# Kernel optimization log

Measured on AMD Instinct MI355X. Metric: run time of the kernel, lower is better.

Reference implementation:

```python
import jax, jax.numpy as jnp
import numpy as np

LAMBDA_TV = 0.01
RHO = 1.0
MAX_ITER = 10
CG_ITER = 10


def _fft2c(x):
    # x: (B, 2, H, W) real/imag stacked -> centered ortho FFT, same layout
    xc = x[:, 0] + 1j * x[:, 1]
    kc = jnp.fft.fftshift(
        jnp.fft.fft2(jnp.fft.ifftshift(xc, axes=(-2, -1)), norm='ortho'),
        axes=(-2, -1))
    return jnp.stack([kc.real, kc.imag], axis=1)


def _ifft2c(x):
    xc = x[:, 0] + 1j * x[:, 1]
    ic = jnp.fft.fftshift(
        jnp.fft.ifft2(jnp.fft.ifftshift(xc, axes=(-2, -1)), norm='ortho'),
        axes=(-2, -1))
    return jnp.stack([ic.real, ic.imag], axis=1)


def _gradient(x):
    # forward differences, zero at the far boundary; cat along channel dim
    dx = jnp.concatenate([x[..., 1:] - x[..., :-1], jnp.zeros_like(x[..., :1])], axis=-1)
    dy = jnp.concatenate([x[..., 1:, :] - x[..., :-1, :], jnp.zeros_like(x[..., :1, :])], axis=-2)
    return jnp.concatenate([dx, dy], axis=1)


def _divergence(p):
    # Faithful to the original: only uses channels 0 and 1 of p -> (B,1,H,W)
    px, py = p[:, 0:1], p[:, 1:2]
    div_x = jnp.concatenate(
        [px[..., 0:1], px[..., 1:-1] - px[..., :-2], -px[..., -2:-1]], axis=-1)
    div_y = jnp.concatenate(
        [py[..., 0:1, :], py[..., 1:-1, :] - py[..., :-2, :], -py[..., -2:-1, :]], axis=-2)
    return div_x + div_y


def soft_threshold(x, t):
    return jnp.sign(x) * jnp.maximum(jnp.abs(x) - t, 0.0)


def _cg_solve(x0, b, mask):
    # Solves (F^H M F + rho * D^H D) x = b with early-stop semantics of the original
    def A(z):
        return _ifft2c(mask * _fft2c(z)) - RHO * _divergence(_gradient(z))

    r0 = b - A(x0)
    rsold0 = jnp.sum(r0 * r0)

    def step(carry, _):
        x, r, p, rsold, done = carry
        Ap = A(p)
        alpha = rsold / (jnp.sum(p * Ap) + 1e-12)
        xn = x + alpha * p
        rn = r - alpha * Ap
        rsnew = jnp.sum(rn * rn)
        stop = rsnew < 1e-10
        pn = rn + (rsnew / rsold) * p
        x = jnp.where(done, x, xn)
        r = jnp.where(done, r, rn)
        p = jnp.where(done | stop, p, pn)
        rsold = jnp.where(done | stop, rsold, rsnew)
        done = done | stop
        return (x, r, p, rsold, done), None

    init = (x0, r0, r0, rsold0, jnp.array(False))
    (x, _, _, _, _), _ = jax.lax.scan(step, init, None, length=CG_ITER)
    return x


def reference(y, mask):
    x0 = _ifft2c(y)
    u0 = _gradient(x0)
    v0 = jnp.zeros_like(u0)
    b_data = _ifft2c(mask * y)  # constant across outer iterations
    thresh = LAMBDA_TV / RHO

    def step(carry, _):
        x, u, v, done, count, pres_l, dres_l = carry
        b = b_data + RHO * _divergence(u - v)
        xn = _cg_solve(x, b, mask)
        g = _gradient(xn)
        un = soft_threshold(g + v, thresh)
        vn = v + g - un
        pres = jnp.linalg.norm(g - un)
        dres = jnp.linalg.norm(RHO * _divergence(un - u))
        stop = (pres < 1e-4) & (dres < 1e-4)
        x = jnp.where(done, x, xn)
        u = jnp.where(done, u, un)
        v = jnp.where(done, v, vn)
        pres_l = jnp.where(done, pres_l, pres)
        dres_l = jnp.where(done, dres_l, dres)
        count = count + (1 - done.astype(jnp.int32))
        done = done | stop
        return (x, u, v, done, count, pres_l, dres_l), None

    init = (x0, u0, v0, jnp.array(False), jnp.array(0, jnp.int32),
            jnp.array(0.0, x0.dtype), jnp.array(0.0, x0.dtype))
    (x, _, _, _, count, pres, dres), _ = jax.lax.scan(step, init, None, length=MAX_ITER)
    return x, count, pres, dres


def setup_inputs() -> dict:
    key = jax.random.key(0)
    k1, k2 = jax.random.split(key)
    B, H, W = 4, 320, 320
    y = jax.random.normal(k1, (B, 2, H, W), dtype=jnp.float32)
    mask = (jax.random.uniform(k2, (B, 1, H, W)) < 0.3).astype(jnp.float32)
    return {"y": y, "mask": mask}
```

## Files before the change

### kernel.cpp

```cpp
#include <hip/hip_runtime.h>
#include <math.h>

#define DEVFN __device__ __forceinline__

namespace {

constexpr int NW = 320, NH = 320, NHW = NW * NH, NB = 4;
constexpr int NC2 = 2 * NHW;
constexpr int GRID = NB * NH;
constexpr int NTHR = 320;
constexpr float THRESHc = 0.01f;

struct C2 { float x, y; };
DEVFN C2 cmul(C2 a, C2 b) { return C2{a.x * b.x - a.y * b.y, a.x * b.y + a.y * b.x}; }

template <int SIGN>
DEVFN C2 TW(const float2* tw, int m) {
  float2 t = tw[m];
  return C2{t.x, (SIGN < 0) ? t.y : -t.y};
}

DEVFN int swzcol(int bid) { return (bid & 7) * (GRID / 8) + (bid >> 3); }

DEVFN void wavebar() {
  __builtin_amdgcn_wave_barrier();
  asm volatile("" ::: "memory");
}

template <int SIGN, bool MASKED>
__device__ void fftp(const float2* IN, float2* OUT, float2* SCR, const float2* tw, int t,
                     const float* __restrict__ misRow) {
  const int q = t >> 6, n1 = t & 63;
  float2* lo = SCR + q * 128;
  float2* hi = lo + 64;
  float mval = 1.f;
  if (MASKED) mval = misRow[5 * n1 + q];
  C2 acc;
  {
    float2 v0 = IN[n1];
    acc.x = v0.x; acc.y = v0.y;
#pragma unroll
    for (int n2 = 1; n2 < 5; n2++) {
      float2 v = IN[n1 + 64 * n2];
      C2 w = TW<SIGN>(tw, 64 * ((n2 * q) % 5));
      acc.x += v.x * w.x - v.y * w.y;
      acc.y += v.x * w.y + v.y * w.x;
    }
    acc = cmul(acc, TW<SIGN>(tw, n1 * q));
  }
  lo[n1] = make_float2(acc.x, acc.y);
  wavebar();
  {
    C2 s{0.f, 0.f};
    int rr = n1 & 3, base = n1 >> 2;
#pragma unroll
    for (int p = 0; p < 4; p++) {
      float2 v = lo[base + 16 * p];
      C2 w = TW<SIGN>(tw, 80 * ((p * rr) & 3));
      s.x += v.x * w.x - v.y * w.y;
      s.y += v.x * w.y + v.y * w.x;
    }
    hi[n1] = make_float2(s.x, s.y);
  }
  wavebar();
  {
    C2 s{0.f, 0.f};
    int rr = n1 & 15, base = ((n1 >> 4) << 2) + (n1 & 3);
#pragma unroll
    for (int p = 0; p < 4; p++) {
      float2 v = hi[base + 16 * p];
      C2 w = TW<SIGN>(tw, 20 * ((p * rr) & 15));
      s.x += v.x * w.x - v.y * w.y;
      s.y += v.x * w.y + v.y * w.x;
    }
    lo[n1] = make_float2(s.x, s.y);
  }
  wavebar();
  {
    C2 s{0.f, 0.f};
    int base = n1 & 15;
#pragma unroll
    for (int p = 0; p < 4; p++) {
      float2 v = lo[base + 16 * p];
      C2 w = TW<SIGN>(tw, 5 * ((p * n1) & 63));
      s.x += v.x * w.x - v.y * w.y;
      s.y += v.x * w.y + v.y * w.x;
    }
    acc = s;
  }
  if (MASKED) { acc.x *= mval; acc.y *= mval; }
  OUT[5 * n1 + q] = make_float2(acc.x, acc.y);
  __syncthreads();
}

DEVFN float Gfunc2(const float2* __restrict__ z, int b, int h, int w) {
  const float2* zz = z + b * NHW;
  int hw = h * NW + w;
  float divx, divy;
  if (w == 0) {
    divx = zz[hw + 1].x - zz[hw].x;
  } else if (w < NW - 1) {
    divx = (zz[hw + 1].x - zz[hw].x) - (zz[hw].x - zz[hw - 1].x);
  } else {
    divx = -(zz[hw].x - zz[hw - 1].x);
  }
  if (h == 0) {
    divy = (w < NW - 1) ? zz[hw + 1].y - zz[hw].y : 0.f;
  } else if (h < NH - 1) {
    float a = (w < NW - 1) ? zz[hw + 1].y - zz[hw].y : 0.f;
    float bb = (w < NW - 1) ? zz[hw - NW + 1].y - zz[hw - NW].y : 0.f;
    divy = a - bb;
  } else {
    divy = -((w < NW - 1) ? zz[hw - NW + 1].y - zz[hw - NW].y : 0.f);
  }
  return divx + divy;
}

DEVFN float divUV(const float* __restrict__ u, const float* __restrict__ v, int b, int h, int w) {
  const float* u0 = u + (b * 4 + 0) * NHW; const float* v0 = v + (b * 4 + 0) * NHW;
  const float* u1 = u + (b * 4 + 1) * NHW; const float* v1 = v + (b * 4 + 1) * NHW;
  int hw = h * NW + w;
  float divx, divy;
  if (w == 0)          divx = u0[hw] - v0[hw];
  else if (w < NW - 1) divx = (u0[hw] - v0[hw]) - (u0[hw - 1] - v0[hw - 1]);
  else                 divx = -(u0[hw - 1] - v0[hw - 1]);
  if (h == 0)          divy = u1[hw] - v1[hw];
  else if (h < NH - 1) divy = (u1[hw] - v1[hw]) - (u1[hw - NW] - v1[hw - NW]);
  else                 divy = -(u1[hw - NW] - v1[hw - NW]);
  return divx + divy;
}

DEVFN double shflxd(double v, int m) {
  union { double d; int i[2]; } a; a.d = v;
  a.i[0] = __shfl_xor(a.i[0], m, 64);
  a.i[1] = __shfl_xor(a.i[1], m, 64);
  return a.d;
}
DEVFN double waveRed(double v) {
#pragma unroll
  for (int m = 32; m; m >>= 1) v += shflxd(v, m);
  return v;
}

__device__ double redParts(const double* __restrict__ part, double* sdot, int t) {
  double v = part[t] + part[t + 320] + part[t + 640] + part[t + 960];
  v = waveRed(v);
  if ((t & 63) == 0) sdot[t >> 6] = v;
  __syncthreads();
  double s = sdot[0] + sdot[1] + sdot[2] + sdot[3] + sdot[4];
  __syncthreads();
  return s;
}

__device__ void blockDot1(double a, double* sdot, int t, double* outp) {
  a = waveRed(a);
  if ((t & 63) == 0) sdot[t >> 6] = a;
  __syncthreads();
  if (t == 0) *outp = sdot[0] + sdot[1] + sdot[2] + sdot[3] + sdot[4];
  __syncthreads();
}

__device__ void blockDot3(double a, double b, double c, double* sdot, int t,
                          double* o0, double* o1, double* o2, int bid) {
  a = waveRed(a); b = waveRed(b); c = waveRed(c);
  int wv = t >> 6;
  if ((t & 63) == 0) { sdot[wv * 3] = a; sdot[wv * 3 + 1] = b; sdot[wv * 3 + 2] = c; }
  __syncthreads();
  if (t == 0) {
    double s0 = 0, s1 = 0, s2 = 0;
#pragma unroll
    for (int w2 = 0; w2 < 5; w2++) { s0 += sdot[w2 * 3]; s1 += sdot[w2 * 3 + 1]; s2 += sdot[w2 * 3 + 2]; }
    o0[bid] = s0; o1[bid] = s1; o2[bid] = s2;
  }
  __syncthreads();
}

#define FFTK_SHARED                                     \
  __shared__ float2 sA[320];                            \
  __shared__ float2 sB[320];                            \
  __shared__ float2 sS[640];                            \
  __shared__ float2 stw[320];                           \
  __shared__ double sdot[16];                           \
  (void)sdot;                                           \
  const int t = threadIdx.x;                            \
  const int bid = blockIdx.x;                           \
  stw[t] = twg[t];


__global__ __launch_bounds__(NTHR) void k_init(const float* __restrict__ mask,
                                               float* __restrict__ misT, float2* __restrict__ tw) {
  int t = threadIdx.x, bid = blockIdx.x;
  if (bid == 0) {
    double ang = -2.0 * 3.14159265358979323846 * (double)t / 320.0;
    tw[t] = make_float2((float)cos(ang), (float)sin(ang));
  }
  int i = bid * NTHR + t;
  int b = i / NHW, hw = i % NHW, h = hw / NW, w = hw % NW;
  int hs = (h + 160) % 320, ws = (w + 160) % 320;
  misT[b * NHW + w * NW + h] = mask[b * NHW + hs * NW + ws] * (1.0f / 102400.0f);
}

__global__ __launch_bounds__(NTHR) void k0a(const float* __restrict__ y, const float* __restrict__ mask,
                                            float2* __restrict__ t1, float2* __restrict__ t2,
                                            const float2* __restrict__ twg) {
  FFTK_SHARED
  const int gb = bid / NH, gl = bid % NH;
  const int rowBase = gb * NC2 + gl * NW;
  float sgn = (t & 1) ? -1.f : 1.f;
  sA[t] = make_float2(sgn * y[rowBase + t], sgn * y[rowBase + NHW + t]);
  __syncthreads();
  fftp<1, false>(sA, sB, sS, stw, t, nullptr);
  {
    float2 v = sB[t];
    t1[gb * NHW + gl * NW + t] = make_float2(sgn * v.x, sgn * v.y);
  }
  float m = mask[gb * NHW + gl * NW + t];
  sA[t] = make_float2(sgn * m * y[rowBase + t], sgn * m * y[rowBase + NHW + t]);
  __syncthreads();
  fftp<1, false>(sA, sB, sS, stw, t, nullptr);
  {
    float2 v = sB[t];
    t2[gb * NHW + gl * NW + t] = make_float2(sgn * v.x, sgn * v.y);
  }
}

__global__ __launch_bounds__(NTHR) void k0b(const float2* __restrict__ t1, const float2* __restrict__ t2,
                                            float2* __restrict__ x2, float2* __restrict__ bdata2,
                                            const float2* __restrict__ twg) {
  FFTK_SHARED
  const int wid = swzcol(bid);
  const int gb = wid / NH, gl = wid % NH;
  float sgn = (t & 1) ? -1.f : 1.f;
  {
    float2 v = t1[gb * NHW + t * NW + gl];
    sA[t] = make_float2(sgn * v.x, sgn * v.y);
  }
  __syncthreads();
  fftp<1, false>(sA, sB, sS, stw, t, nullptr);
  {
    float2 v = sB[t];
    float s = sgn * (1.f / 320.f);
    x2[gb * NHW + t * NW + gl] = make_float2(v.x * s, v.y * s);
  }
  {
    float2 v = t2[gb * NHW + t * NW + gl];
    sA[t] = make_float2(sgn * v.x, sgn * v.y);
  }
  __syncthreads();
  fftp<1, false>(sA, sB, sS, stw, t, nullptr);
  {
    float2 v = sB[t];
    float s = sgn * (1.f / 320.f);
    bdata2[gb * NHW + t * NW + gl] = make_float2(v.x * s, v.y * s);
  }
}

__global__ __launch_bounds__(NTHR) void ka0(const float2* __restrict__ x2, float2* __restrict__ xc2,
                                            float* __restrict__ u, float* __restrict__ v,
                                            float2* __restrict__ t1, const float2* __restrict__ twg) {
  FFTK_SHARED
  const int gb = bid / NH, gl = bid % NH;
  {
    int i = bid * NTHR + t;
    int b = i / NHW, hw = i % NHW, h = hw / NW, w = hw % NW;
    const float2* zz = x2 + b * NHW;
    float2 z0 = zz[hw];
    float g0 = 0, g1 = 0, g2 = 0, g3 = 0;
    if (w < NW - 1) { float2 zr = zz[hw + 1]; g0 = zr.x - z0.x; g1 = zr.y - z0.y; }
    if (h < NH - 1) { float2 zd = zz[hw + NW]; g2 = zd.x - z0.x; g3 = zd.y - z0.y; }
    int b4 = b * 4 * NHW;
    u[b4 + hw] = g0;           v[b4 + hw] = 0.f;
    u[b4 + NHW + hw] = g1;     v[b4 + NHW + hw] = 0.f;
    u[b4 + 2 * NHW + hw] = g2; v[b4 + 2 * NHW + hw] = 0.f;
    u[b4 + 3 * NHW + hw] = g3; v[b4 + 3 * NHW + hw] = 0.f;
  }
  int idx = gb * NHW + gl * NW + t;
  float2 xv = x2[idx];
  xc2[idx] = xv;
  sA[t] = xv;
  __syncthreads();
  fftp<-1, false>(sA, sB, sS, stw, t, nullptr);
  t1[idx] = sB[t];
}

__global__ __launch_bounds__(NTHR) void kb(float2* __restrict__ t1, const float* __restrict__ misT,
                                           const float* __restrict__ un, const float* __restrict__ vn,
                                           float* __restrict__ u, float* __restrict__ v,
                                           const double* __restrict__ pPaPrev, const double* __restrict__ pPbPrev,
                                           double* __restrict__ hist_pres, double* __restrict__ hist_dres,
                                           const float2* __restrict__ twg, int it) {
  FFTK_SHARED
  const int wid = swzcol(bid);
  const int gb = wid / NH, gl = wid % NH;
  if (it > 0) {
    double ppa = redParts(pPaPrev, sdot, t);
    double ppb = redParts(pPbPrev, sdot, t);
    if (bid == 0 && t == 0) { hist_pres[it - 1] = ppa; hist_dres[it - 1] = ppb; }
    bool doneA = false;
    for (int j = 0; j <= it - 2; j++) {
      float pr = sqrtf((float)hist_pres[j]), dr = sqrtf((float)hist_dres[j]);
      doneA |= (pr < 1e-4f && dr < 1e-4f);
    }
    if (!doneA) {
      for (int i = wid * NTHR + t; i < NB * 4 * NHW; i += GRID * NTHR) { u[i] = un[i]; v[i] = vn[i]; }
    }
  }
  sA[t] = t1[gb * NHW + t * NW + gl];
  __syncthreads();
  fftp<-1, true>(sA, sB, sS, stw, t, misT + gb * NHW + gl * NW);
  fftp<1, false>(sB, sA, sS, stw, t, nullptr);
  t1[gb * NHW + t * NW + gl] = sA[t];
}

__global__ __launch_bounds__(NTHR) void kcd(float2* __restrict__ t1, const float2* __restrict__ x2,
                                            const float* __restrict__ u, const float* __restrict__ v,
                                            const float2* __restrict__ bdata2, float2* __restrict__ r2,
                                            float2* __restrict__ p2, double* __restrict__ pRS,
                                            const float2* __restrict__ twg) {
  FFTK_SHARED
  const int gb = bid / NH, gl = bid % NH;
  const int idx = gb * NHW + gl * NW + t;
  sA[t] = t1[idx];
  __syncthreads();
  fftp<1, false>(sA, sB, sS, stw, t, nullptr);
  float2 Av = sB[t];
  float G = Gfunc2(x2, gb, gl, t);
  float d = divUV(u, v, gb, gl, t);
  float2 bd = bdata2[idx];
  float rr = (bd.x + d) - (Av.x - G);
  float ri = (bd.y + d) - (Av.y - G);
  float2 rv = make_float2(rr, ri);
  r2[idx] = rv; p2[idx] = rv;
  double acc = (double)rr * rr + (double)ri * ri;
  blockDot1(acc, sdot, t, &pRS[bid]);
  sA[t] = rv;
  __syncthreads();
  fftp<-1, false>(sA, sB, sS, stw, t, nullptr);
  t1[idx] = sB[t];
}

__global__ __launch_bounds__(NTHR) void kd(float2* __restrict__ xc2, float2* __restrict__ r2,
                                           float2* __restrict__ p2, const float2* __restrict__ Ap2,
                                           float2* __restrict__ t1, const double* __restrict__ pRS,
                                           const double* __restrict__ pD0, const double* __restrict__ pD1,
                                           const double* __restrict__ pD2, double* __restrict__ hist_rs,
                                           const float2* __restrict__ twg, int k) {
  FFTK_SHARED
  const int gb = bid / NH, gl = bid % NH;
  const int idx = gb * NHW + gl * NW + t;
  double pAp = redParts(pD0, sdot, t);
  double rAp = redParts(pD1, sdot, t);
  double A2  = redParts(pD2, sdot, t);
  double rsold = (k == 1) ? redParts(pRS, sdot, t) : hist_rs[k - 2];
  float alpha = (float)rsold / ((float)pAp + 1e-12f);
  double rsnew = rsold - 2.0 * (double)alpha * rAp + (double)alpha * (double)alpha * A2;
  if (bid == 0 && t == 0) hist_rs[k - 1] = rsnew;
  bool doneIn = false;
  for (int j = 0; j <= k - 2; j++) doneIn |= ((float)hist_rs[j] < 1e-10f);
  bool stop = ((float)rsnew < 1e-10f);
  bool doneP = doneIn || stop;
  float beta = (float)rsnew / (float)rsold;
  float2 pv = p2[idx], rv = r2[idx], av = Ap2[idx], xv = xc2[idx];
  if (!doneIn) {
    xv.x += alpha * pv.x; xv.y += alpha * pv.y;
    rv.x -= alpha * av.x; rv.y -= alpha * av.y;
  }
  float2 pn = doneP ? pv : make_float2(rv.x + beta * pv.x, rv.y + beta * pv.y);
  xc2[idx] = xv; r2[idx] = rv; p2[idx] = pn;
  sA[t] = pn;
  __syncthreads();
  fftp<-1, false>(sA, sB, sS, stw, t, nullptr);
  t1[idx] = sB[t];
}

__global__ __launch_bounds__(NTHR) void ke(float2* __restrict__ t1, const float* __restrict__ misT,
                                           const float2* __restrict__ twg) {
  FFTK_SHARED
  const int wid = swzcol(bid);
  const int gb = wid / NH, gl = wid % NH;
  sA[t] = t1[gb * NHW + t * NW + gl];
  __syncthreads();
  fftp<-1, true>(sA, sB, sS, stw, t, misT + gb * NHW + gl * NW);
  fftp<1, false>(sB, sA, sS, stw, t, nullptr);
  t1[gb * NHW + t * NW + gl] = sA[t];
}

__global__ __launch_bounds__(NTHR) void kf(const float2* __restrict__ t1, const float2* __restrict__ p2,
                                           const float2* __restrict__ r2, float2* __restrict__ Ap2,
                                           double* __restrict__ pD0, double* __restrict__ pD1,
                                           double* __restrict__ pD2, const float2* __restrict__ twg) {
  FFTK_SHARED
  const int gb = bid / NH, gl = bid % NH;
  const int idx = gb * NHW + gl * NW + t;
  sA[t] = t1[idx];
  __syncthreads();
  fftp<1, false>(sA, sB, sS, stw, t, nullptr);
  float2 Av = sB[t];
  float G = Gfunc2(p2, gb, gl, t);
  float Ar = Av.x - G, Ai = Av.y - G;
  Ap2[idx] = make_float2(Ar, Ai);
  float2 pv = p2[idx], rv = r2[idx];
  double aP = (double)pv.x * Ar + (double)pv.y * Ai;
  double aR = (double)rv.x * Ar + (double)rv.y * Ai;
  double aA = (double)Ar * Ar + (double)Ai * Ai;
  blockDot3(aP, aR, aA, sdot, t, pD0, pD1, pD2, bid);
}

__global__ __launch_bounds__(NTHR) void kh1(const float2* __restrict__ xc2, const float2* __restrict__ p2,
                                            const float* __restrict__ v, float2* __restrict__ t1,
                                            float* __restrict__ un, float* __restrict__ vn,
                                            const double* __restrict__ pD0, const double* __restrict__ hist_rs,
                                            double* __restrict__ pPaCur) {
  __shared__ double sdot[16];
  const int t = threadIdx.x, bid = blockIdx.x;
  double pAp = redParts(pD0, sdot, t);
  double rsold = hist_rs[8];
  float alphaF = (float)rsold / ((float)pAp + 1e-12f);
  bool doneX = false;
  for (int j = 0; j <= 8; j++) doneX |= ((float)hist_rs[j] < 1e-10f);
  int i = bid * NTHR + t;
  int b = i / NHW, hw = i % NHW, h = hw / NW, w = hw % NW;
  int base2 = b * NHW;
  auto XN = [&](int off) {
    float2 vv = xc2[base2 + off];
    if (!doneX) {
      float2 pp = p2[base2 + off];
      vv.x += alphaF * pp.x; vv.y += alphaF * pp.y;
    }
    return vv;
  };
  float2 x0 = XN(hw);
  float g0 = 0, g1 = 0, g2 = 0, g3 = 0;
  if (w < NW - 1) { float2 xr = XN(hw + 1); g0 = xr.x - x0.x; g1 = xr.y - x0.y; }
  if (h < NH - 1) { float2 xd = XN(hw + NW); g2 = xd.x - x0.x; g3 = xd.y - x0.y; }
  t1[base2 + hw] = x0;
  float gs[4] = {g0, g1, g2, g3};
  double acc = 0.0;
#pragma unroll
  for (int ch = 0; ch < 4; ch++) {
    int ui = (b * 4 + ch) * NHW + hw;
    float vv = v[ui];
    float sv = gs[ch] + vv;
    float a2 = fabsf(sv) - THRESHc;
    float uo = (a2 > 0.f) ? copysignf(a2, sv) : 0.f;
    un[ui] = uo;
    vn[ui] = vv + gs[ch] - uo;
    float dd = gs[ch] - uo;
    acc += (double)dd * dd;
  }
  blockDot1(acc, sdot, t, &pPaCur[bid]);
}

__global__ __launch_bounds__(NTHR) void kh2a(float2* __restrict__ x2, float2* __restrict__ xc2,
                                             float2* __restrict__ t1, const float* __restrict__ un,
                                             const float* __restrict__ u,
                                             const double* __restrict__ hist_pres,
                                             const double* __restrict__ hist_dres,
                                             double* __restrict__ pPbCur,
                                             const float2* __restrict__ twg, int it) {
  FFTK_SHARED
  const int gb = bid / NH, gl = bid % NH;
  const int idx = gb * NHW + gl * NW + t;
  bool doneA = false;
  for (int j = 0; j <= it - 1; j++) {
    float pr = sqrtf((float)hist_pres[j]), dr = sqrtf((float)hist_dres[j]);
    doneA |= (pr < 1e-4f && dr < 1e-4f);
  }
  {
    int i = bid * NTHR + t;
    int b = i / NHW, hw = i % NHW, h = hw / NW, w = hw % NW;
    const float* N0 = un + (b * 4 + 0) * NHW; const float* U0 = u + (b * 4 + 0) * NHW;
    const float* N1 = un + (b * 4 + 1) * NHW; const float* U1 = u + (b * 4 + 1) * NHW;
    float divx, divy;
    if (w == 0)          divx = N0[hw] - U0[hw];
    else if (w < NW - 1) divx = (N0[hw] - U0[hw]) - (N0[hw - 1] - U0[hw - 1]);
    else                 divx = -(N0[hw - 1] - U0[hw - 1]);
    if (h == 0)          divy = N1[hw] - U1[hw];
    else if (h < NH - 1) divy = (N1[hw] - U1[hw]) - (N1[hw - NW] - U1[hw - NW]);
    else                 divy = -(N1[hw - NW] - U1[hw - NW]);
    float d = divx + divy;
    double acc = (double)d * d;
    blockDot1(acc, sdot, t, &pPbCur[bid]);
  }
  float2 xn = t1[idx];
  float2 xf = doneA ? x2[idx] : xn;
  x2[idx] = xf; xc2[idx] = xf;
  sA[t] = xf;
  __syncthreads();
  fftp<-1, false>(sA, sB, sS, stw, t, nullptr);
  t1[idx] = sB[t];
}

__global__ __launch_bounds__(NTHR) void k_out(const float2* __restrict__ x2,
                                              const double* __restrict__ hist_pres,
                                              const double* __restrict__ hist_dres,
                                              const double* __restrict__ pPa9,
                                              const double* __restrict__ pPb9,
                                              float* __restrict__ out) {
  __shared__ double sdot[16];
  const int t = threadIdx.x, bid = blockIdx.x;
  {
    int i = bid * NTHR + t;
    int b = i / NHW, hw = i % NHW;
    float2 v = x2[b * NHW + hw];
    out[b * NC2 + hw] = v.x;
    out[b * NC2 + NHW + hw] = v.y;
  }
  if (bid == 0) {
    double p9 = redParts(pPa9, sdot, t);
    double d9 = redParts(pPb9, sdot, t);
    if (t == 0) {
      int count = 0; bool done = false; float presO = 0.f, dresO = 0.f;
      for (int it = 0; it < 10; ++it) {
        double hp = (it == 9) ? p9 : hist_pres[it];
        double hd = (it == 9) ? d9 : hist_dres[it];
        if (!done) {
          count++;
          presO = sqrtf((float)hp);
          dresO = sqrtf((float)hd);
          done = (presO < 1e-4f) && (dresO < 1e-4f);
        }
      }
      out[NB * NC2 + 0] = (float)count;
      out[NB * NC2 + 1] = presO;
      out[NB * NC2 + 2] = dresO;
    }
  }
}

}

extern "C" void kernel_launch(void* const* d_in, const int* in_sizes, int n_in,
                              void* d_out, int out_size, void* d_ws, size_t ws_size,
                              hipStream_t stream) {
  (void)in_sizes; (void)n_in; (void)out_size; (void)ws_size;
  const float* y = (const float*)d_in[0];
  const float* mask = (const float*)d_in[1];
  float* out = (float*)d_out;
  float* wsf = (float*)d_ws;

  double* dws = (double*)wsf;
  double* pRS       = dws;
  double* pD0       = dws + 1280;
  double* pD1       = dws + 2560;
  double* pD2       = dws + 3840;
  double* pPa       = dws + 5120;
  double* pPb       = dws + 7680;
  double* hist_rs   = dws + 10240;
  double* hist_pres = dws + 10256;
  double* hist_dres = dws + 10272;

  float* fb = wsf + 20576;
  float2* tw = (float2*)fb; fb += 640;
  float* misT = fb; fb += (size_t)NB * NHW;
  float2* t1 = (float2*)fb; fb += (size_t)2 * NB * NHW;
  float2* t2 = (float2*)fb; fb += (size_t)2 * NB * NHW;
  auto take2 = [&](size_t n) { float2* ptr = (float2*)fb; fb += 2 * n; return ptr; };
  float2* x2     = take2((size_t)NB * NHW);
  float2* xc2    = take2((size_t)NB * NHW);
  float2* r2     = take2((size_t)NB * NHW);
  float2* p2     = take2((size_t)NB * NHW);
  float2* Ap2    = take2((size_t)NB * NHW);
  float2* bdata2 = take2((size_t)NB * NHW);
  auto take = [&](size_t n) { float* ptr = fb; fb += n; return ptr; };
  float* u  = take((size_t)NB * 4 * NHW);
  float* v  = take((size_t)NB * 4 * NHW);
  float* un = take((size_t)NB * 4 * NHW);
  float* vn = take((size_t)NB * 4 * NHW);

  k_init<<<GRID, NTHR, 0, stream>>>(mask, misT, tw);
  k0a<<<GRID, NTHR, 0, stream>>>(y, mask, t1, t2, tw);
  k0b<<<GRID, NTHR, 0, stream>>>(t1, t2, x2, bdata2, tw);
  ka0<<<GRID, NTHR, 0, stream>>>(x2, xc2, u, v, t1, tw);

  for (int it = 0; it < 10; ++it) {
    int prevPar = (it + 1) & 1;
    int curPar = it & 1;
    kb<<<GRID, NTHR, 0, stream>>>(t1, misT, un, vn, u, v,
                                  pPa + prevPar * 1280, pPb + prevPar * 1280,
                                  hist_pres, hist_dres, tw, it);
    kcd<<<GRID, NTHR, 0, stream>>>(t1, x2, u, v, bdata2, r2, p2, pRS, tw);
    ke<<<GRID, NTHR, 0, stream>>>(t1, misT, tw);
    kf<<<GRID, NTHR, 0, stream>>>(t1, p2, r2, Ap2, pD0, pD1, pD2, tw);
    for (int k = 1; k < 10; ++k) {
      kd<<<GRID, NTHR, 0, stream>>>(xc2, r2, p2, Ap2, t1, pRS, pD0, pD1, pD2, hist_rs, tw, k);
      ke<<<GRID, NTHR, 0, stream>>>(t1, misT, tw);
      kf<<<GRID, NTHR, 0, stream>>>(t1, p2, r2, Ap2, pD0, pD1, pD2, tw);
    }
    kh1<<<GRID, NTHR, 0, stream>>>(xc2, p2, v, t1, un, vn, pD0, hist_rs, pPa + curPar * 1280);
    kh2a<<<GRID, NTHR, 0, stream>>>(x2, xc2, t1, un, u, hist_pres, hist_dres,
                                    pPb + curPar * 1280, tw, it);
  }
  k_out<<<GRID, NTHR, 0, stream>>>(x2, hist_pres, hist_dres, pPa + 1280, pPb + 1280, out);
}
```

Before: 2.933 ms.

## Transpose FFT intermediates on write to make column-pass reads row-contiguous

Intermediate spectra are now written transposed by the row-FFT kernels, so the following column-FFT kernels read contiguous rows instead of strided columns. The single in-place buffer t1 becomes two ping-pong buffers tA/tB to avoid read-write hazards between transposed layouts, and more kernels use the swizzled block index. This moves the strided access from reads to writes, which may coalesce better or worse depending on write-combining behavior.

```diff
diff --git a/kernel.cpp b/kernel.cpp
--- a/kernel.cpp
+++ b/kernel.cpp
@@ -187,6 +187,7 @@
   stw[t] = twg[t];
 
 
+
 __global__ __launch_bounds__(NTHR) void k_init(const float* __restrict__ mask,
                                                float* __restrict__ misT, float2* __restrict__ tw) {
   int t = threadIdx.x, bid = blockIdx.x;
@@ -201,10 +202,11 @@
 }
 
 __global__ __launch_bounds__(NTHR) void k0a(const float* __restrict__ y, const float* __restrict__ mask,
-                                            float2* __restrict__ t1, float2* __restrict__ t2,
+                                            float2* __restrict__ tA, float2* __restrict__ tB,
                                             const float2* __restrict__ twg) {
   FFTK_SHARED
-  const int gb = bid / NH, gl = bid % NH;
+  const int wid = swzcol(bid);
+  const int gb = wid / NH, gl = wid % NH;
   const int rowBase = gb * NC2 + gl * NW;
   float sgn = (t & 1) ? -1.f : 1.f;
   sA[t] = make_float2(sgn * y[rowBase + t], sgn * y[rowBase + NHW + t]);
@@ -212,7 +214,7 @@
   fftp<1, false>(sA, sB, sS, stw, t, nullptr);
   {
     float2 v = sB[t];
-    t1[gb * NHW + gl * NW + t] = make_float2(sgn * v.x, sgn * v.y);
+    tA[gb * NHW + t * NW + gl] = make_float2(sgn * v.x, sgn * v.y);
   }
   float m = mask[gb * NHW + gl * NW + t];
   sA[t] = make_float2(sgn * m * y[rowBase + t], sgn * m * y[rowBase + NHW + t]);
@@ -220,11 +222,11 @@
   fftp<1, false>(sA, sB, sS, stw, t, nullptr);
   {
     float2 v = sB[t];
-    t2[gb * NHW + gl * NW + t] = make_float2(sgn * v.x, sgn * v.y);
-  }
-}
-
-__global__ __launch_bounds__(NTHR) void k0b(const float2* __restrict__ t1, const float2* __restrict__ t2,
+    tB[gb * NHW + t * NW + gl] = make_float2(sgn * v.x, sgn * v.y);
+  }
+}
+
+__global__ __launch_bounds__(NTHR) void k0b(const float2* __restrict__ tA, const float2* __restrict__ tB,
                                             float2* __restrict__ x2, float2* __restrict__ bdata2,
                                             const float2* __restrict__ twg) {
   FFTK_SHARED
@@ -232,7 +234,7 @@
   const int gb = wid / NH, gl = wid % NH;
   float sgn = (t & 1) ? -1.f : 1.f;
   {
-    float2 v = t1[gb * NHW + t * NW + gl];
+    float2 v = tA[gb * NHW + gl * NW + t];
     sA[t] = make_float2(sgn * v.x, sgn * v.y);
   }
   __syncthreads();
@@ -243,7 +245,7 @@
     x2[gb * NHW + t * NW + gl] = make_float2(v.x * s, v.y * s);
   }
   {
-    float2 v = t2[gb * NHW + t * NW + gl];
+    float2 v = tB[gb * NHW + gl * NW + t];
     sA[t] = make_float2(sgn * v.x, sgn * v.y);
   }
   __syncthreads();
@@ -257,9 +259,10 @@
 
 __global__ __launch_bounds__(NTHR) void ka0(const float2* __restrict__ x2, float2* __restrict__ xc2,
                                             float* __restrict__ u, float* __restrict__ v,
-                                            float2* __restrict__ t1, const float2* __restrict__ twg) {
-  FFTK_SHARED
-  const int gb = bid / NH, gl = bid % NH;
+                                            float2* __restrict__ tA, const float2* __restrict__ twg) {
+  FFTK_SHARED
+  const int wid = swzcol(bid);
+  const int gb = wid / NH, gl = wid % NH;
   {
     int i = bid * NTHR + t;
     int b = i / NHW, hw = i % NHW, h = hw / NW, w = hw % NW;
@@ -280,10 +283,11 @@
   sA[t] = xv;
   __syncthreads();
   fftp<-1, false>(sA, sB, sS, stw, t, nullptr);
-  t1[idx] = sB[t];
-}
-
-__global__ __launch_bounds__(NTHR) void kb(float2* __restrict__ t1, const float* __restrict__ misT,
+  tA[gb * NHW + t * NW + gl] = sB[t];
+}
+
+__global__ __launch_bounds__(NTHR) void kb(const float2* __restrict__ tA, float2* __restrict__ tB,
+                                           const float* __restrict__ misT,
                                            const float* __restrict__ un, const float* __restrict__ vn,
                                            float* __restrict__ u, float* __restrict__ v,
                                            const double* __restrict__ pPaPrev, const double* __restrict__ pPbPrev,
@@ -305,22 +309,24 @@
       for (int i = wid * NTHR + t; i < NB * 4 * NHW; i += GRID * NTHR) { u[i] = un[i]; v[i] = vn[i]; }
     }
   }
-  sA[t] = t1[gb * NHW + t * NW + gl];
+  sA[t] = tA[gb * NHW + gl * NW + t];
   __syncthreads();
   fftp<-1, true>(sA, sB, sS, stw, t, misT + gb * NHW + gl * NW);
   fftp<1, false>(sB, sA, sS, stw, t, nullptr);
-  t1[gb * NHW + t * NW + gl] = sA[t];
-}
-
-__global__ __launch_bounds__(NTHR) void kcd(float2* __restrict__ t1, const float2* __restrict__ x2,
+  tB[gb * NHW + t * NW + gl] = sA[t];
+}
+
+__global__ __launch_bounds__(NTHR) void kcd(const float2* __restrict__ tB, float2* __restrict__ tA,
+                                            const float2* __restrict__ x2,
                                             const float* __restrict__ u, const float* __restrict__ v,
                                             const float2* __restrict__ bdata2, float2* __restrict__ r2,
                                             float2* __restrict__ p2, double* __restrict__ pRS,
                                             const float2* __restrict__ twg) {
   FFTK_SHARED
-  const int gb = bid / NH, gl = bid % NH;
+  const int wid = swzcol(bid);
+  const int gb = wid / NH, gl = wid % NH;
   const int idx = gb * NHW + gl * NW + t;
-  sA[t] = t1[idx];
+  sA[t] = tB[idx];
   __syncthreads();
   fftp<1, false>(sA, sB, sS, stw, t, nullptr);
   float2 Av = sB[t];
@@ -336,17 +342,18 @@
   sA[t] = rv;
   __syncthreads();
   fftp<-1, false>(sA, sB, sS, stw, t, nullptr);
-  t1[idx] = sB[t];
+  tA[gb * NHW + t * NW + gl] = sB[t];
 }
 
 __global__ __launch_bounds__(NTHR) void kd(float2* __restrict__ xc2, float2* __restrict__ r2,
                                            float2* __restrict__ p2, const float2* __restrict__ Ap2,
-                                           float2* __restrict__ t1, const double* __restrict__ pRS,
+                                           float2* __restrict__ tA, const double* __restrict__ pRS,
                                            const double* __restrict__ pD0, const double* __restrict__ pD1,
                                            const double* __restrict__ pD2, double* __restrict__ hist_rs,
                                            const float2* __restrict__ twg, int k) {
   FFTK_SHARED
-  const int gb = bid / NH, gl = bid % NH;
+  const int wid = swzcol(bid);
+  const int gb = wid / NH, gl = wid % NH;
   const int idx = gb * NHW + gl * NW + t;
   double pAp = redParts(pD0, sdot, t);
   double rAp = redParts(pD1, sdot, t);
@@ -370,29 +377,31 @@
   sA[t] = pn;
   __syncthreads();
   fftp<-1, false>(sA, sB, sS, stw, t, nullptr);
-  t1[idx] = sB[t];
-}
-
-__global__ __launch_bounds__(NTHR) void ke(float2* __restrict__ t1, const float* __restrict__ misT,
+  tA[gb * NHW + t * NW + gl] = sB[t];
+}
+
+__global__ __launch_bounds__(NTHR) void ke(const float2* __restrict__ tA, float2* __restrict__ tB,
+                                           const float* __restrict__ misT,
                                            const float2* __restrict__ twg) {
   FFTK_SHARED
   const int wid = swzcol(bid);
   const int gb = wid / NH, gl = wid % NH;
-  sA[t] = t1[gb * NHW + t * NW + gl];
+  sA[t] = tA[gb * NHW + gl * NW + t];
   __syncthreads();
   fftp<-1, true>(sA, sB, sS, stw, t, misT + gb * NHW + gl * NW);
   fftp<1, false>(sB, sA, sS, stw, t, nullptr);
-  t1[gb * NHW + t * NW + gl] = sA[t];
-}
-
-__global__ __launch_bounds__(NTHR) void kf(const float2* __restrict__ t1, const float2* __restrict__ p2,
+  tB[gb * NHW + t * NW + gl] = sA[t];
+}
+
+__global__ __launch_bounds__(NTHR) void kf(const float2* __restrict__ tB, const float2* __restrict__ p2,
                                            const float2* __restrict__ r2, float2* __restrict__ Ap2,
                                            double* __restrict__ pD0, double* __restrict__ pD1,
                                            double* __restrict__ pD2, const float2* __restrict__ twg) {
   FFTK_SHARED
-  const int gb = bid / NH, gl = bid % NH;
+  const int wid = swzcol(bid);
+  const int gb = wid / NH, gl = wid % NH;
   const int idx = gb * NHW + gl * NW + t;
-  sA[t] = t1[idx];
+  sA[t] = tB[idx];
   __syncthreads();
   fftp<1, false>(sA, sB, sS, stw, t, nullptr);
   float2 Av = sB[t];
@@ -407,7 +416,7 @@
 }
 
 __global__ __launch_bounds__(NTHR) void kh1(const float2* __restrict__ xc2, const float2* __restrict__ p2,
-                                            const float* __restrict__ v, float2* __restrict__ t1,
+                                            const float* __restrict__ v, float2* __restrict__ tB,
                                             float* __restrict__ un, float* __restrict__ vn,
                                             const double* __restrict__ pD0, const double* __restrict__ hist_rs,
                                             double* __restrict__ pPaCur) {
@@ -433,7 +442,7 @@
   float g0 = 0, g1 = 0, g2 = 0, g3 = 0;
   if (w < NW - 1) { float2 xr = XN(hw + 1); g0 = xr.x - x0.x; g1 = xr.y - x0.y; }
   if (h < NH - 1) { float2 xd = XN(hw + NW); g2 = xd.x - x0.x; g3 = xd.y - x0.y; }
-  t1[base2 + hw] = x0;
+  tB[base2 + hw] = x0;
   float gs[4] = {g0, g1, g2, g3};
   double acc = 0.0;
 #pragma unroll
@@ -452,14 +461,16 @@
 }
 
 __global__ __launch_bounds__(NTHR) void kh2a(float2* __restrict__ x2, float2* __restrict__ xc2,
-                                             float2* __restrict__ t1, const float* __restrict__ un,
+                                             const float2* __restrict__ tB, float2* __restrict__ tA,
+                                             const float* __restrict__ un,
                                              const float* __restrict__ u,
                                              const double* __restrict__ hist_pres,
                                              const double* __restrict__ hist_dres,
                                              double* __restrict__ pPbCur,
                                              const float2* __restrict__ twg, int it) {
   FFTK_SHARED
-  const int gb = bid / NH, gl = bid % NH;
+  const int wid = swzcol(bid);
+  const int gb = wid / NH, gl = wid % NH;
   const int idx = gb * NHW + gl * NW + t;
   bool doneA = false;
   for (int j = 0; j <= it - 1; j++) {
@@ -482,13 +493,13 @@
     double acc = (double)d * d;
     blockDot1(acc, sdot, t, &pPbCur[bid]);
   }
-  float2 xn = t1[idx];
+  float2 xn = tB[idx];
   float2 xf = doneA ? x2[idx] : xn;
   x2[idx] = xf; xc2[idx] = xf;
   sA[t] = xf;
   __syncthreads();
   fftp<-1, false>(sA, sB, sS, stw, t, nullptr);
-  t1[idx] = sB[t];
+  tA[gb * NHW + t * NW + gl] = sB[t];
 }
 
 __global__ __launch_bounds__(NTHR) void k_out(const float2* __restrict__ x2,
@@ -553,8 +564,8 @@
   float* fb = wsf + 20576;
   float2* tw = (float2*)fb; fb += 640;
   float* misT = fb; fb += (size_t)NB * NHW;
-  float2* t1 = (float2*)fb; fb += (size_t)2 * NB * NHW;
-  float2* t2 = (float2*)fb; fb += (size_t)2 * NB * NHW;
+  float2* tA = (float2*)fb; fb += (size_t)2 * NB * NHW;
+  float2* tB = (float2*)fb; fb += (size_t)2 * NB * NHW;
   auto take2 = [&](size_t n) { float2* ptr = (float2*)fb; fb += 2 * n; return ptr; };
   float2* x2     = take2((size_t)NB * NHW);
   float2* xc2    = take2((size_t)NB * NHW);
@@ -569,26 +580,26 @@
   float* vn = take((size_t)NB * 4 * NHW);
 
   k_init<<<GRID, NTHR, 0, stream>>>(mask, misT, tw);
-  k0a<<<GRID, NTHR, 0, stream>>>(y, mask, t1, t2, tw);
-  k0b<<<GRID, NTHR, 0, stream>>>(t1, t2, x2, bdata2, tw);
-  ka0<<<GRID, NTHR, 0, stream>>>(x2, xc2, u, v, t1, tw);
+  k0a<<<GRID, NTHR, 0, stream>>>(y, mask, tA, tB, tw);
+  k0b<<<GRID, NTHR, 0, stream>>>(tA, tB, x2, bdata2, tw);
+  ka0<<<GRID, NTHR, 0, stream>>>(x2, xc2, u, v, tA, tw);
 
   for (int it = 0; it < 10; ++it) {
     int prevPar = (it + 1) & 1;
     int curPar = it & 1;
-    kb<<<GRID, NTHR, 0, stream>>>(t1, misT, un, vn, u, v,
+    kb<<<GRID, NTHR, 0, stream>>>(tA, tB, misT, un, vn, u, v,
                                   pPa + prevPar * 1280, pPb + prevPar * 1280,
                                   hist_pres, hist_dres, tw, it);
-    kcd<<<GRID, NTHR, 0, stream>>>(t1, x2, u, v, bdata2, r2, p2, pRS, tw);
-    ke<<<GRID, NTHR, 0, stream>>>(t1, misT, tw);
-    kf<<<GRID, NTHR, 0, stream>>>(t1, p2, r2, Ap2, pD0, pD1, pD2, tw);
+    kcd<<<GRID, NTHR, 0, stream>>>(tB, tA, x2, u, v, bdata2, r2, p2, pRS, tw);
+    ke<<<GRID, NTHR, 0, stream>>>(tA, tB, misT, tw);
+    kf<<<GRID, NTHR, 0, stream>>>(tB, p2, r2, Ap2, pD0, pD1, pD2, tw);
     for (int k = 1; k < 10; ++k) {
-      kd<<<GRID, NTHR, 0, stream>>>(xc2, r2, p2, Ap2, t1, pRS, pD0, pD1, pD2, hist_rs, tw, k);
-      ke<<<GRID, NTHR, 0, stream>>>(t1, misT, tw);
-      kf<<<GRID, NTHR, 0, stream>>>(t1, p2, r2, Ap2, pD0, pD1, pD2, tw);
-    }
-    kh1<<<GRID, NTHR, 0, stream>>>(xc2, p2, v, t1, un, vn, pD0, hist_rs, pPa + curPar * 1280);
-    kh2a<<<GRID, NTHR, 0, stream>>>(x2, xc2, t1, un, u, hist_pres, hist_dres,
+      kd<<<GRID, NTHR, 0, stream>>>(xc2, r2, p2, Ap2, tA, pRS, pD0, pD1, pD2, hist_rs, tw, k);
+      ke<<<GRID, NTHR, 0, stream>>>(tA, tB, misT, tw);
+      kf<<<GRID, NTHR, 0, stream>>>(tB, p2, r2, Ap2, pD0, pD1, pD2, tw);
+    }
+    kh1<<<GRID, NTHR, 0, stream>>>(xc2, p2, v, tB, un, vn, pD0, hist_rs, pPa + curPar * 1280);
+    kh2a<<<GRID, NTHR, 0, stream>>>(x2, xc2, tB, tA, un, u, hist_pres, hist_dres,
                                     pPb + curPar * 1280, tw, it);
   }
   k_out<<<GRID, NTHR, 0, stream>>>(x2, hist_pres, hist_dres, pPa + 1280, pPb + 1280, out);
```

Result: faster. 2.822 ms (-3.8%).
